# Kernel optimization log

Hardware: AMD Instinct MI355X
Metric: run time of the kernel (lower is better)

Reference implementation:

```python
import jax, jax.numpy as jnp
import numpy as np

EMBED = 256
B, S = 4, 4096

def _linear_params(key, d):
    k1, k2 = jax.random.split(key)
    lim = 1.0 / np.sqrt(d)
    W = jax.random.uniform(k1, (d, d), jnp.float32, -lim, lim)
    b = jax.random.uniform(k2, (d,), jnp.float32, -lim, lim)
    return W, b

def setup_inputs() -> dict:
    key = jax.random.key(0)
    ks = jax.random.split(key, 6)
    x = jax.random.normal(ks[0], (B, S, EMBED), jnp.float32)
    Wq, bq = _linear_params(ks[1], EMBED)
    Wk, bk = _linear_params(ks[2], EMBED)
    Wv, bv = _linear_params(ks[3], EMBED)
    Wl, bl = _linear_params(ks[4], EMBED)
    g1 = jnp.ones((EMBED,), jnp.float32); be1 = jnp.zeros((EMBED,), jnp.float32)
    g2 = jnp.ones((EMBED,), jnp.float32); be2 = jnp.zeros((EMBED,), jnp.float32)
    return {"x": x, "Wq": Wq, "bq": bq, "Wk": Wk, "bk": bk, "Wv": Wv, "bv": bv,
            "Wl": Wl, "bl": bl, "g1": g1, "be1": be1, "g2": g2, "be2": be2}

def _layernorm(x, g, b, eps=1e-5):
    mu = jnp.mean(x, axis=-1, keepdims=True)
    var = jnp.mean(jnp.square(x - mu), axis=-1, keepdims=True)
    return (x - mu) * jax.lax.rsqrt(var + eps) * g + b

def reference(x, Wq, bq, Wk, bk, Wv, bv, Wl, bl, g1, be1, g2, be2):
    d = x.shape[-1]
    q = jnp.einsum('bsd,ed->bse', x, Wq) + bq
    k = jnp.einsum('bsd,ed->bse', x, Wk) + bk
    v = jnp.einsum('bsd,ed->bse', x, Wv) + bv
    scores = jnp.einsum('bqd,bkd->bqk', q, k) / np.sqrt(d).astype(np.float32)
    attn = jax.nn.softmax(scores, axis=-1)
    out = jnp.einsum('bqk,bkd->bqd', attn, v)
    h = _layernorm(x + out, g1, be1)
    # NOTE: same linear applied twice (as in the original module)
    h = jnp.einsum('bsd,ed->bse', h, Wl) + bl
    h = jax.nn.relu(h)
    h = jnp.einsum('bsd,ed->bse', h, Wl) + bl
    return _layernorm(x + h, g2, be2)
```

## Files before the change

kernel.cpp:

```cpp
#include <hip/hip_runtime.h>

typedef unsigned short u16;
typedef float  f32x4 __attribute__((ext_vector_type(4)));
typedef short  s16x8 __attribute__((ext_vector_type(8)));
typedef unsigned short u16x4 __attribute__((ext_vector_type(4)));

__device__ __forceinline__ u16 f2b(float f) {
    unsigned b = __float_as_uint(f);
    return (u16)((b + 0x7FFFu + ((b >> 16) & 1u)) >> 16);
}
__device__ __forceinline__ float b2f(u16 u) { return __uint_as_float(((unsigned)u) << 16); }

__device__ __forceinline__ int perm64(int r) {
    return (r & 0x23) | (((r >> 2) & 3) << 3) | (((r >> 4) & 1) << 2);
}

__device__ __forceinline__ void gload16(const u16* g, u16* l) {
    __builtin_amdgcn_global_load_lds(
        (const __attribute__((address_space(1))) unsigned int*)g,
        (__attribute__((address_space(3))) unsigned int*)l,
        16, 0, 0);
}

__global__ __launch_bounds__(256) void cvt_f2b_k(const float* __restrict__ src, u16* __restrict__ dst, int n) {
    int i = (blockIdx.x * 256 + threadIdx.x) * 4;
    if (i < n) {
        f32x4 v = *(const f32x4*)(src + i);
        u16x4 o;
        o[0] = f2b(v[0]); o[1] = f2b(v[1]); o[2] = f2b(v[2]); o[3] = f2b(v[3]);
        *(u16x4*)(dst + i) = o;
    }
}

template<int TRANS, int RELU>
__global__ __launch_bounds__(256) void gemm_k256(const u16* __restrict__ A, const u16* __restrict__ W,
                                                 const float* __restrict__ bias, u16* __restrict__ Cd,
                                                 float scale) {
    const int tid = threadIdx.x;
    const int wv = tid >> 6, lane = tid & 63, g = lane >> 4, lq = lane & 15;
    const int m0 = blockIdx.x * 64, n0 = blockIdx.y * 64;

    const u16* arow = A + (size_t)(m0 + wv * 16 + lq) * 256;
    f32x4 acc[4];
#pragma unroll
    for (int nf = 0; nf < 4; ++nf) { acc[nf][0] = 0.f; acc[nf][1] = 0.f; acc[nf][2] = 0.f; acc[nf][3] = 0.f; }

#pragma unroll
    for (int kk = 0; kk < 8; ++kk) {
        s16x8 a = *(const s16x8*)(arow + kk * 32 + g * 8);
#pragma unroll
        for (int nf = 0; nf < 4; ++nf) {
            s16x8 b = *(const s16x8*)(W + (size_t)(n0 + nf * 16 + lq) * 256 + kk * 32 + g * 8);
            acc[nf] = __builtin_amdgcn_mfma_f32_16x16x32_bf16(a, b, acc[nf], 0, 0, 0);
        }
    }

    __shared__ __align__(16) u16 c_lds[64 * 64];
#pragma unroll
    for (int nf = 0; nf < 4; ++nf) {
        float bb = bias[n0 + nf * 16 + lq];
#pragma unroll
        for (int j = 0; j < 4; ++j) {
            float v = acc[nf][j] + bb;
            if (RELU) v = fmaxf(v, 0.f);
            v *= scale;
            if (!TRANS) c_lds[(wv * 16 + (g << 2) + j) * 64 + nf * 16 + lq] = f2b(v);
            else        c_lds[(nf * 16 + lq) * 64 + wv * 16 + (g << 2) + j] = f2b(v);
        }
    }
    __syncthreads();
    if (!TRANS) {
#pragma unroll
        for (int r = 0; r < 2; ++r) {
            int o = (r * 256 + tid) * 8, row = o >> 6, col = o & 63;
            *(s16x8*)(Cd + (size_t)(m0 + row) * 256 + n0 + col) = *(const s16x8*)(c_lds + row * 64 + col);
        }
    } else {
        int bidx = m0 >> 12, s0 = m0 & 4095;
#pragma unroll
        for (int r = 0; r < 2; ++r) {
            int o = (r * 256 + tid) * 8, drow = o >> 6, col = o & 63;
            *(s16x8*)(Cd + (size_t)bidx * 256 * 4096 + (size_t)(n0 + drow) * 4096 + s0 + col) =
                *(const s16x8*)(c_lds + drow * 64 + col);
        }
    }
}

__global__ __launch_bounds__(256, 1) void flash2(const u16* __restrict__ Q, const u16* __restrict__ K,
                                                 const u16* __restrict__ VT, u16* __restrict__ Opart,
                                                 float* __restrict__ ml) {
    __shared__ __align__(16) u16 smem[65536];
    const int tid = threadIdx.x;
    const int wv = tid >> 6, lane = tid & 63, g = lane >> 4, lqi = lane & 15;
    const int bx = blockIdx.x, s = blockIdx.y;
    const int b = bx >> 5, q0 = (bx & 31) << 7;
    const int kvbase = s * 2048;

    const u16* kb_ = K + (size_t)b * 4096 * 256;
    const u16* vb_ = VT + (size_t)b * 256 * 4096;

    s16x8 qf[2][8];
#pragma unroll
    for (int qh = 0; qh < 2; ++qh) {
        const u16* qrow = Q + (size_t)(b * 4096 + q0 + wv * 32 + qh * 16 + lqi) * 256;
#pragma unroll
        for (int kk = 0; kk < 8; ++kk) qf[qh][kk] = *(const s16x8*)(qrow + kk * 32 + g * 8);
    }

    int koff[8], voff[8];
#pragma unroll
    for (int r = 0; r < 8; ++r) {
        int row = r * 8 + (tid >> 5), ch = tid & 31;
        koff[r] = perm64(row) * 256 + ((ch ^ (row & 7)) << 3);
        int vrow = r * 32 + (tid >> 3), vch = tid & 7;
        voff[r] = vrow * 4096 + ((vch ^ (vrow & 7)) << 3);
    }

    f32x4 acc[2][16];
#pragma unroll
    for (int qh = 0; qh < 2; ++qh)
#pragma unroll
        for (int nf = 0; nf < 16; ++nf) { acc[qh][nf][0]=0.f; acc[qh][nf][1]=0.f; acc[qh][nf][2]=0.f; acc[qh][nf][3]=0.f; }
    float mrun[2] = {-1e30f, -1e30f}, lrun[2] = {0.f, 0.f};

    auto STAGE = [&](int bufsel, int t) {
        const u16* kt = kb_ + (size_t)(kvbase + (t << 6)) * 256;
        const u16* vt = vb_ + (kvbase + (t << 6));
        u16* kl = smem + bufsel * 32768 + tid * 8;
        u16* vl = kl + 16384;
#pragma unroll
        for (int r = 0; r < 8; ++r) gload16(kt + koff[r], kl + r * 2048);
#pragma unroll
        for (int r = 0; r < 8; ++r) gload16(vt + voff[r], vl + r * 2048);
    };

    auto COMPUTE = [&](int bufsel) {
        const u16* kbuf = smem + bufsel * 32768;
        const u16* vbuf = kbuf + 16384;
        f32x4 st[2][4];
#pragma unroll
        for (int qh = 0; qh < 2; ++qh)
#pragma unroll
            for (int f = 0; f < 4; ++f) { st[qh][f][0]=0.f; st[qh][f][1]=0.f; st[qh][f][2]=0.f; st[qh][f][3]=0.f; }
#pragma unroll
        for (int kk = 0; kk < 8; ++kk) {
#pragma unroll
            for (int f = 0; f < 4; ++f) {
                int row = f * 16 + lqi;
                s16x8 a = *(const s16x8*)(kbuf + ((row << 5) + (((kk << 2) + g) ^ (row & 7))) * 8);
                st[0][f] = __builtin_amdgcn_mfma_f32_16x16x32_bf16(a, qf[0][kk], st[0][f], 0, 0, 0);
                st[1][f] = __builtin_amdgcn_mfma_f32_16x16x32_bf16(a, qf[1][kk], st[1][f], 0, 0, 0);
            }
        }
        s16x8 pa[2][2];
#pragma unroll
        for (int qh = 0; qh < 2; ++qh) {
            float rm = -1e30f;
#pragma unroll
            for (int f = 0; f < 4; ++f)
                rm = fmaxf(rm, fmaxf(fmaxf(st[qh][f][0], st[qh][f][1]), fmaxf(st[qh][f][2], st[qh][f][3])));
            rm = fmaxf(rm, __shfl_xor(rm, 16));
            rm = fmaxf(rm, __shfl_xor(rm, 32));
            if (!__all(rm - mrun[qh] <= 8.f)) {
                float mnew = fmaxf(mrun[qh], rm);
                float alpha = exp2f(mrun[qh] - mnew);
#pragma unroll
                for (int j = 0; j < 4; ++j) {
                    float a4 = __shfl(alpha, (g << 2) + j);
#pragma unroll
                    for (int nf = 0; nf < 16; ++nf) acc[qh][nf][j] *= a4;
                }
                mrun[qh] = mnew;
                lrun[qh] *= alpha;
            }
            float ps = 0.f;
#pragma unroll
            for (int f = 0; f < 4; ++f)
#pragma unroll
                for (int j = 0; j < 4; ++j) { float e = exp2f(st[qh][f][j] - mrun[qh]); st[qh][f][j] = e; ps += e; }
            ps += __shfl_xor(ps, 16);
            ps += __shfl_xor(ps, 32);
            lrun[qh] += ps;
#pragma unroll
            for (int kk2 = 0; kk2 < 2; ++kk2) {
                union { s16x8 v; u16 u[8]; } pu;
#pragma unroll
                for (int j2 = 0; j2 < 4; ++j2) { pu.u[j2] = f2b(st[qh][2*kk2][j2]); pu.u[4+j2] = f2b(st[qh][2*kk2+1][j2]); }
                pa[qh][kk2] = pu.v;
            }
        }
#pragma unroll
        for (int kk2 = 0; kk2 < 2; ++kk2) {
#pragma unroll
            for (int nf = 0; nf < 16; ++nf) {
                int row = (nf << 4) + lqi;
                s16x8 bv = *(const s16x8*)(vbuf + ((row << 3) + (((kk2 << 2) + g) ^ (row & 7))) * 8);
                acc[0][nf] = __builtin_amdgcn_mfma_f32_16x16x32_bf16(pa[0][kk2], bv, acc[0][nf], 0, 0, 0);
                acc[1][nf] = __builtin_amdgcn_mfma_f32_16x16x32_bf16(pa[1][kk2], bv, acc[1][nf], 0, 0, 0);
            }
        }
    };

    STAGE(0, 0);
    for (int t2 = 0; t2 < 32; t2 += 2) {
        __syncthreads();
        STAGE(1, t2 + 1);
        COMPUTE(0);
        __syncthreads();
        if (t2 + 2 < 32) STAGE(0, t2 + 2);
        COMPUTE(1);
    }

    __syncthreads();
    float linv[2][4];
#pragma unroll
    for (int qh = 0; qh < 2; ++qh)
#pragma unroll
        for (int j = 0; j < 4; ++j) linv[qh][j] = 1.0f / __shfl(lrun[qh], (g << 2) + j);
    u16* o_lds = smem;
#pragma unroll
    for (int qh = 0; qh < 2; ++qh)
#pragma unroll
        for (int nf = 0; nf < 16; ++nf)
#pragma unroll
            for (int j = 0; j < 4; ++j)
                o_lds[(wv * 32 + qh * 16 + (g << 2) + j) * 256 + (nf << 4) + lqi] = f2b(acc[qh][nf][j] * linv[qh][j]);
    __syncthreads();
    u16* orow = Opart + (size_t)s * 4194304 + (size_t)(b * 4096 + q0) * 256;
#pragma unroll
    for (int r = 0; r < 16; ++r) {
        int o = (r * 256 + tid) * 8, row = o >> 8, col = o & 255;
        *(s16x8*)(orow + (size_t)row * 256 + col) = *(const s16x8*)(o_lds + row * 256 + col);
    }
    if (lane < 16) {
#pragma unroll
        for (int qh = 0; qh < 2; ++qh) {
            int grow = b * 4096 + q0 + wv * 32 + qh * 16 + lqi;
            ml[s * 32768 + grow]         = mrun[qh];
            ml[s * 32768 + 16384 + grow] = lrun[qh];
        }
    }
}

__global__ __launch_bounds__(256) void recomb_k(const u16* __restrict__ Opart, const float* __restrict__ ml,
                                                u16* __restrict__ out) {
    const int row = blockIdx.x * 4 + (threadIdx.x >> 6);
    const int lane = threadIdx.x & 63;
    float m0 = ml[row],          l0 = ml[16384 + row];
    float m1 = ml[32768 + row],  l1 = ml[49152 + row];
    float mm = fmaxf(m0, m1);
    float a0 = l0 * exp2f(m0 - mm), a1 = l1 * exp2f(m1 - mm);
    float rs = 1.0f / (a0 + a1);
    a0 *= rs; a1 *= rs;
    u16x4 v0 = *(const u16x4*)(Opart + (size_t)row * 256 + lane * 4);
    u16x4 v1 = *(const u16x4*)(Opart + 4194304 + (size_t)row * 256 + lane * 4);
    u16x4 o;
#pragma unroll
    for (int i = 0; i < 4; ++i) o[i] = f2b(a0 * b2f(v0[i]) + a1 * b2f(v1[i]));
    *(u16x4*)(out + (size_t)row * 256 + lane * 4) = o;
}

template<int OUTF32>
__global__ __launch_bounds__(256) void ln_k(const float* __restrict__ x, const u16* __restrict__ add,
                                            const float* __restrict__ gam, const float* __restrict__ bet,
                                            float* __restrict__ outf, u16* __restrict__ outb) {
    const int row = blockIdx.x * 4 + (threadIdx.x >> 6);
    const int lane = threadIdx.x & 63;
    f32x4 xv = *(const f32x4*)(x + (size_t)row * 256 + lane * 4);
    u16x4 av = *(const u16x4*)(add + (size_t)row * 256 + lane * 4);
    float s[4];
#pragma unroll
    for (int i = 0; i < 4; ++i) s[i] = xv[i] + b2f(av[i]);
    float sum = s[0] + s[1] + s[2] + s[3];
    float sq = s[0] * s[0] + s[1] * s[1] + s[2] * s[2] + s[3] * s[3];
#pragma unroll
    for (int d = 1; d < 64; d <<= 1) { sum += __shfl_xor(sum, d); sq += __shfl_xor(sq, d); }
    float mean = sum * (1.f / 256.f);
    float var = sq * (1.f / 256.f) - mean * mean;
    float rstd = rsqrtf(var + 1e-5f);
    f32x4 gv = *(const f32x4*)(gam + lane * 4);
    f32x4 bv = *(const f32x4*)(bet + lane * 4);
    if (OUTF32) {
        f32x4 y;
#pragma unroll
        for (int i = 0; i < 4; ++i) y[i] = (s[i] - mean) * rstd * gv[i] + bv[i];
        *(f32x4*)(outf + (size_t)row * 256 + lane * 4) = y;
    } else {
        u16x4 y;
#pragma unroll
        for (int i = 0; i < 4; ++i) y[i] = f2b((s[i] - mean) * rstd * gv[i] + bv[i]);
        *(u16x4*)(outb + (size_t)row * 256 + lane * 4) = y;
    }
}

extern "C" void kernel_launch(void* const* d_in, const int* in_sizes, int n_in,
                              void* d_out, int out_size, void* d_ws, size_t ws_size,
                              hipStream_t stream) {
    const float* x   = (const float*)d_in[0];
    const float* Wq  = (const float*)d_in[1];
    const float* bq  = (const float*)d_in[2];
    const float* Wk  = (const float*)d_in[3];
    const float* bk  = (const float*)d_in[4];
    const float* Wv  = (const float*)d_in[5];
    const float* bv  = (const float*)d_in[6];
    const float* Wl  = (const float*)d_in[7];
    const float* bl  = (const float*)d_in[8];
    const float* g1  = (const float*)d_in[9];
    const float* be1 = (const float*)d_in[10];
    const float* g2  = (const float*)d_in[11];
    const float* be2 = (const float*)d_in[12];
    float* out = (float*)d_out;

    const size_t NT = 16384 * 256;
    u16* xb  = (u16*)d_ws;
    u16* qb  = xb  + NT;
    u16* kb  = qb  + NT;
    u16* vtb = kb  + NT;
    u16* o01 = vtb + NT;
    u16* wqb = o01 + 2 * NT;
    u16* wkb = wqb + 65536;
    u16* wvb = wkb + 65536;
    u16* wlb = wvb + 65536;
    float* ml = (float*)(wlb + 65536);

    cvt_f2b_k<<<4096, 256, 0, stream>>>(x, xb, 4194304);
    cvt_f2b_k<<<64, 256, 0, stream>>>(Wq, wqb, 65536);
    cvt_f2b_k<<<64, 256, 0, stream>>>(Wk, wkb, 65536);
    cvt_f2b_k<<<64, 256, 0, stream>>>(Wv, wvb, 65536);
    cvt_f2b_k<<<64, 256, 0, stream>>>(Wl, wlb, 65536);

    dim3 ggrid(256, 4);
    gemm_k256<0, 0><<<ggrid, 256, 0, stream>>>(xb, wqb, bq, qb, 0.0625f * 1.44269504f);
    gemm_k256<0, 0><<<ggrid, 256, 0, stream>>>(xb, wkb, bk, kb, 1.0f);
    gemm_k256<1, 0><<<ggrid, 256, 0, stream>>>(xb, wvb, bv, vtb, 1.0f);

    flash2<<<dim3(128, 2), 256, 0, stream>>>(qb, kb, vtb, o01, ml);
    recomb_k<<<4096, 256, 0, stream>>>(o01, ml, xb );

    ln_k<0><<<4096, 256, 0, stream>>>(x, xb, g1, be1, nullptr, qb );

    gemm_k256<0, 1><<<ggrid, 256, 0, stream>>>(qb, wlb, bl, kb , 1.0f);
    gemm_k256<0, 0><<<ggrid, 256, 0, stream>>>(kb, wlb, bl, vtb , 1.0f);

    ln_k<1><<<4096, 256, 0, stream>>>(x, vtb, g2, be2, out, nullptr);
}
```

Measured before the change: 371.1 us.

## Fuse QKV projection with x conversion, widen flash blocks, add split-K variants

```diff
diff --git a/kernel.cpp b/kernel.cpp
--- a/kernel.cpp
+++ b/kernel.cpp
@@ -4,6 +4,8 @@
 typedef float  f32x4 __attribute__((ext_vector_type(4)));
 typedef short  s16x8 __attribute__((ext_vector_type(8)));
 typedef unsigned short u16x4 __attribute__((ext_vector_type(4)));
+
+#define NT 4194304
 
 __device__ __forceinline__ u16 f2b(float f) {
     unsigned b = __float_as_uint(f);
@@ -22,29 +24,95 @@
         16, 0, 0);
 }
 
-__global__ __launch_bounds__(256) void cvt_f2b_k(const float* __restrict__ src, u16* __restrict__ dst, int n) {
+__global__ __launch_bounds__(256) void cvt_w4(const float* __restrict__ w0, const float* __restrict__ w1,
+                                              const float* __restrict__ w2, const float* __restrict__ w3,
+                                              u16* __restrict__ dst) {
+    const int z = blockIdx.y;
+    const float* src = z == 0 ? w0 : z == 1 ? w1 : z == 2 ? w2 : w3;
     int i = (blockIdx.x * 256 + threadIdx.x) * 4;
-    if (i < n) {
-        f32x4 v = *(const f32x4*)(src + i);
-        u16x4 o;
-        o[0] = f2b(v[0]); o[1] = f2b(v[1]); o[2] = f2b(v[2]); o[3] = f2b(v[3]);
-        *(u16x4*)(dst + i) = o;
-    }
-}
-
-template<int TRANS, int RELU>
+    f32x4 v = *(const f32x4*)(src + i);
+    u16x4 o;
+    o[0] = f2b(v[0]); o[1] = f2b(v[1]); o[2] = f2b(v[2]); o[3] = f2b(v[3]);
+    *(u16x4*)(dst + (size_t)z * 65536 + i) = o;
+}
+
+__global__ __launch_bounds__(256) void gemm_qkv(const float* __restrict__ x, const u16* __restrict__ wqkv,
+                                                const float* __restrict__ bq, const float* __restrict__ bk,
+                                                const float* __restrict__ bv,
+                                                u16* __restrict__ q, u16* __restrict__ k, u16* __restrict__ vt,
+                                                float qscale) {
+    const int tid = threadIdx.x;
+    const int wid = tid >> 6, lane = tid & 63, g = lane >> 4, lq = lane & 15;
+    const int m0 = blockIdx.x * 64, n0 = blockIdx.y * 64, z = blockIdx.z;
+    const u16* W = wqkv + (size_t)z * 65536;
+    const float* bias = z == 0 ? bq : z == 1 ? bk : bv;
+    const float scale = z == 0 ? qscale : 1.0f;
+
+    const float* arow = x + (size_t)(m0 + wid * 16 + lq) * 256;
+    s16x8 af[8];
+#pragma unroll
+    for (int kk = 0; kk < 8; ++kk) {
+        f32x4 lo = *(const f32x4*)(arow + kk * 32 + g * 8);
+        f32x4 hi = *(const f32x4*)(arow + kk * 32 + g * 8 + 4);
+        union { s16x8 v; u16 u[8]; } pu;
+#pragma unroll
+        for (int e = 0; e < 4; ++e) { pu.u[e] = f2b(lo[e]); pu.u[4 + e] = f2b(hi[e]); }
+        af[kk] = pu.v;
+    }
+
+    f32x4 acc[4];
+#pragma unroll
+    for (int nf = 0; nf < 4; ++nf) { acc[nf][0]=0.f; acc[nf][1]=0.f; acc[nf][2]=0.f; acc[nf][3]=0.f; }
+#pragma unroll
+    for (int kk = 0; kk < 8; ++kk) {
+#pragma unroll
+        for (int nf = 0; nf < 4; ++nf) {
+            s16x8 b = *(const s16x8*)(W + (size_t)(n0 + nf * 16 + lq) * 256 + kk * 32 + g * 8);
+            acc[nf] = __builtin_amdgcn_mfma_f32_16x16x32_bf16(af[kk], b, acc[nf], 0, 0, 0);
+        }
+    }
+
+    __shared__ __align__(16) u16 c_lds[64 * 64];
+#pragma unroll
+    for (int nf = 0; nf < 4; ++nf) {
+        float bb = bias[n0 + nf * 16 + lq];
+#pragma unroll
+        for (int j = 0; j < 4; ++j) {
+            float v = (acc[nf][j] + bb) * scale;
+            if (z != 2) c_lds[(wid * 16 + (g << 2) + j) * 64 + nf * 16 + lq] = f2b(v);
+            else        c_lds[(nf * 16 + lq) * 64 + wid * 16 + (g << 2) + j] = f2b(v);
+        }
+    }
+    __syncthreads();
+    if (z != 2) {
+        u16* Cd = z == 0 ? q : k;
+#pragma unroll
+        for (int r = 0; r < 2; ++r) {
+            int o = (r * 256 + tid) * 8, row = o >> 6, col = o & 63;
+            *(s16x8*)(Cd + (size_t)(m0 + row) * 256 + n0 + col) = *(const s16x8*)(c_lds + row * 64 + col);
+        }
+    } else {
+        int bidx = m0 >> 12, s0 = m0 & 4095;
+#pragma unroll
+        for (int r = 0; r < 2; ++r) {
+            int o = (r * 256 + tid) * 8, drow = o >> 6, col = o & 63;
+            *(s16x8*)(vt + (size_t)bidx * 1048576 + (size_t)(n0 + drow) * 4096 + s0 + col) =
+                *(const s16x8*)(c_lds + drow * 64 + col);
+        }
+    }
+}
+
+template<int RELU>
 __global__ __launch_bounds__(256) void gemm_k256(const u16* __restrict__ A, const u16* __restrict__ W,
-                                                 const float* __restrict__ bias, u16* __restrict__ Cd,
-                                                 float scale) {
+                                                 const float* __restrict__ bias, u16* __restrict__ Cd) {
     const int tid = threadIdx.x;
-    const int wv = tid >> 6, lane = tid & 63, g = lane >> 4, lq = lane & 15;
+    const int wid = tid >> 6, lane = tid & 63, g = lane >> 4, lq = lane & 15;
     const int m0 = blockIdx.x * 64, n0 = blockIdx.y * 64;
 
-    const u16* arow = A + (size_t)(m0 + wv * 16 + lq) * 256;
+    const u16* arow = A + (size_t)(m0 + wid * 16 + lq) * 256;
     f32x4 acc[4];
 #pragma unroll
-    for (int nf = 0; nf < 4; ++nf) { acc[nf][0] = 0.f; acc[nf][1] = 0.f; acc[nf][2] = 0.f; acc[nf][3] = 0.f; }
-
+    for (int nf = 0; nf < 4; ++nf) { acc[nf][0]=0.f; acc[nf][1]=0.f; acc[nf][2]=0.f; acc[nf][3]=0.f; }
 #pragma unroll
     for (int kk = 0; kk < 8; ++kk) {
         s16x8 a = *(const s16x8*)(arow + kk * 32 + g * 8);
@@ -54,7 +122,6 @@
             acc[nf] = __builtin_amdgcn_mfma_f32_16x16x32_bf16(a, b, acc[nf], 0, 0, 0);
         }
     }
-
     __shared__ __align__(16) u16 c_lds[64 * 64];
 #pragma unroll
     for (int nf = 0; nf < 4; ++nf) {
@@ -63,38 +130,25 @@
         for (int j = 0; j < 4; ++j) {
             float v = acc[nf][j] + bb;
             if (RELU) v = fmaxf(v, 0.f);
-            v *= scale;
-            if (!TRANS) c_lds[(wv * 16 + (g << 2) + j) * 64 + nf * 16 + lq] = f2b(v);
-            else        c_lds[(nf * 16 + lq) * 64 + wv * 16 + (g << 2) + j] = f2b(v);
+            c_lds[(wid * 16 + (g << 2) + j) * 64 + nf * 16 + lq] = f2b(v);
         }
     }
     __syncthreads();
-    if (!TRANS) {
-#pragma unroll
-        for (int r = 0; r < 2; ++r) {
-            int o = (r * 256 + tid) * 8, row = o >> 6, col = o & 63;
-            *(s16x8*)(Cd + (size_t)(m0 + row) * 256 + n0 + col) = *(const s16x8*)(c_lds + row * 64 + col);
-        }
-    } else {
-        int bidx = m0 >> 12, s0 = m0 & 4095;
-#pragma unroll
-        for (int r = 0; r < 2; ++r) {
-            int o = (r * 256 + tid) * 8, drow = o >> 6, col = o & 63;
-            *(s16x8*)(Cd + (size_t)bidx * 256 * 4096 + (size_t)(n0 + drow) * 4096 + s0 + col) =
-                *(const s16x8*)(c_lds + drow * 64 + col);
-        }
-    }
-}
-
-__global__ __launch_bounds__(256, 1) void flash2(const u16* __restrict__ Q, const u16* __restrict__ K,
+#pragma unroll
+    for (int r = 0; r < 2; ++r) {
+        int o = (r * 256 + tid) * 8, row = o >> 6, col = o & 63;
+        *(s16x8*)(Cd + (size_t)(m0 + row) * 256 + n0 + col) = *(const s16x8*)(c_lds + row * 64 + col);
+    }
+}
+
+__global__ __launch_bounds__(512, 2) void flash3(const u16* __restrict__ Q, const u16* __restrict__ K,
                                                  const u16* __restrict__ VT, u16* __restrict__ Opart,
-                                                 float* __restrict__ ml) {
+                                                 float* __restrict__ ml, int ntiles) {
     __shared__ __align__(16) u16 smem[65536];
     const int tid = threadIdx.x;
-    const int wv = tid >> 6, lane = tid & 63, g = lane >> 4, lqi = lane & 15;
-    const int bx = blockIdx.x, s = blockIdx.y;
-    const int b = bx >> 5, q0 = (bx & 31) << 7;
-    const int kvbase = s * 2048;
+    const int wid = tid >> 6, lane = tid & 63, g = lane >> 4, lqi = lane & 15;
+    const int b = blockIdx.x >> 4, q0 = (blockIdx.x & 15) << 8;
+    const int s = blockIdx.y, kvbase = s * (ntiles << 6);
 
     const u16* kb_ = K + (size_t)b * 4096 * 256;
     const u16* vb_ = VT + (size_t)b * 256 * 4096;
@@ -102,17 +156,18 @@
     s16x8 qf[2][8];
 #pragma unroll
     for (int qh = 0; qh < 2; ++qh) {
-        const u16* qrow = Q + (size_t)(b * 4096 + q0 + wv * 32 + qh * 16 + lqi) * 256;
+        const u16* qrow = Q + (size_t)(b * 4096 + q0 + wid * 32 + qh * 16 + lqi) * 256;
 #pragma unroll
         for (int kk = 0; kk < 8; ++kk) qf[qh][kk] = *(const s16x8*)(qrow + kk * 32 + g * 8);
     }
 
-    int koff[8], voff[8];
-#pragma unroll
-    for (int r = 0; r < 8; ++r) {
-        int row = r * 8 + (tid >> 5), ch = tid & 31;
+    int koff[4], voff[4];
+#pragma unroll
+    for (int r = 0; r < 4; ++r) {
+        int c = r * 512 + tid;
+        int row = c >> 5, ch = c & 31;
         koff[r] = perm64(row) * 256 + ((ch ^ (row & 7)) << 3);
-        int vrow = r * 32 + (tid >> 3), vch = tid & 7;
+        int vrow = c >> 3, vch = c & 7;
         voff[r] = vrow * 4096 + ((vch ^ (vrow & 7)) << 3);
     }
 
@@ -126,12 +181,12 @@
     auto STAGE = [&](int bufsel, int t) {
         const u16* kt = kb_ + (size_t)(kvbase + (t << 6)) * 256;
         const u16* vt = vb_ + (kvbase + (t << 6));
-        u16* kl = smem + bufsel * 32768 + tid * 8;
+        u16* kl = smem + bufsel * 32768;
         u16* vl = kl + 16384;
 #pragma unroll
-        for (int r = 0; r < 8; ++r) gload16(kt + koff[r], kl + r * 2048);
-#pragma unroll
-        for (int r = 0; r < 8; ++r) gload16(vt + voff[r], vl + r * 2048);
+        for (int r = 0; r < 4; ++r) gload16(kt + koff[r], kl + (r * 512 + tid) * 8);
+#pragma unroll
+        for (int r = 0; r < 4; ++r) gload16(vt + voff[r], vl + (r * 512 + tid) * 8);
     };
 
     auto COMPUTE = [&](int bufsel) {
@@ -142,6 +197,7 @@
         for (int qh = 0; qh < 2; ++qh)
 #pragma unroll
             for (int f = 0; f < 4; ++f) { st[qh][f][0]=0.f; st[qh][f][1]=0.f; st[qh][f][2]=0.f; st[qh][f][3]=0.f; }
+        __builtin_amdgcn_s_setprio(1);
 #pragma unroll
         for (int kk = 0; kk < 8; ++kk) {
 #pragma unroll
@@ -152,6 +208,7 @@
                 st[1][f] = __builtin_amdgcn_mfma_f32_16x16x32_bf16(a, qf[1][kk], st[1][f], 0, 0, 0);
             }
         }
+        __builtin_amdgcn_s_setprio(0);
         s16x8 pa[2][2];
 #pragma unroll
         for (int qh = 0; qh < 2; ++qh) {
@@ -189,6 +246,7 @@
                 pa[qh][kk2] = pu.v;
             }
         }
+        __builtin_amdgcn_s_setprio(1);
 #pragma unroll
         for (int kk2 = 0; kk2 < 2; ++kk2) {
 #pragma unroll
@@ -199,15 +257,16 @@
                 acc[1][nf] = __builtin_amdgcn_mfma_f32_16x16x32_bf16(pa[1][kk2], bv, acc[1][nf], 0, 0, 0);
             }
         }
+        __builtin_amdgcn_s_setprio(0);
     };
 
     STAGE(0, 0);
-    for (int t2 = 0; t2 < 32; t2 += 2) {
+    for (int t2 = 0; t2 < ntiles; t2 += 2) {
         __syncthreads();
         STAGE(1, t2 + 1);
         COMPUTE(0);
         __syncthreads();
-        if (t2 + 2 < 32) STAGE(0, t2 + 2);
+        if (t2 + 2 < ntiles) STAGE(0, t2 + 2);
         COMPUTE(1);
     }
 
@@ -224,39 +283,47 @@
         for (int nf = 0; nf < 16; ++nf)
 #pragma unroll
             for (int j = 0; j < 4; ++j)
-                o_lds[(wv * 32 + qh * 16 + (g << 2) + j) * 256 + (nf << 4) + lqi] = f2b(acc[qh][nf][j] * linv[qh][j]);
+                o_lds[(wid * 32 + qh * 16 + (g << 2) + j) * 256 + (nf << 4) + lqi] = f2b(acc[qh][nf][j] * linv[qh][j]);
     __syncthreads();
-    u16* orow = Opart + (size_t)s * 4194304 + (size_t)(b * 4096 + q0) * 256;
+    u16* orow = Opart + (size_t)s * NT + (size_t)(b * 4096 + q0) * 256;
 #pragma unroll
     for (int r = 0; r < 16; ++r) {
-        int o = (r * 256 + tid) * 8, row = o >> 8, col = o & 255;
+        int o = (r * 512 + tid) * 8, row = o >> 8, col = o & 255;
         *(s16x8*)(orow + (size_t)row * 256 + col) = *(const s16x8*)(o_lds + row * 256 + col);
     }
     if (lane < 16) {
 #pragma unroll
         for (int qh = 0; qh < 2; ++qh) {
-            int grow = b * 4096 + q0 + wv * 32 + qh * 16 + lqi;
+            int grow = b * 4096 + q0 + wid * 32 + qh * 16 + lqi;
             ml[s * 32768 + grow]         = mrun[qh];
             ml[s * 32768 + 16384 + grow] = lrun[qh];
         }
     }
 }
 
+template<int S>
 __global__ __launch_bounds__(256) void recomb_k(const u16* __restrict__ Opart, const float* __restrict__ ml,
                                                 u16* __restrict__ out) {
     const int row = blockIdx.x * 4 + (threadIdx.x >> 6);
     const int lane = threadIdx.x & 63;
-    float m0 = ml[row],          l0 = ml[16384 + row];
-    float m1 = ml[32768 + row],  l1 = ml[49152 + row];
-    float mm = fmaxf(m0, m1);
-    float a0 = l0 * exp2f(m0 - mm), a1 = l1 * exp2f(m1 - mm);
-    float rs = 1.0f / (a0 + a1);
-    a0 *= rs; a1 *= rs;
-    u16x4 v0 = *(const u16x4*)(Opart + (size_t)row * 256 + lane * 4);
-    u16x4 v1 = *(const u16x4*)(Opart + 4194304 + (size_t)row * 256 + lane * 4);
-    u16x4 o;
-#pragma unroll
-    for (int i = 0; i < 4; ++i) o[i] = f2b(a0 * b2f(v0[i]) + a1 * b2f(v1[i]));
+    float m[S], l[S];
+#pragma unroll
+    for (int s = 0; s < S; ++s) { m[s] = ml[s * 32768 + row]; l[s] = ml[s * 32768 + 16384 + row]; }
+    float mm = m[0];
+#pragma unroll
+    for (int s = 1; s < S; ++s) mm = fmaxf(mm, m[s]);
+    float a[S], tot = 0.f;
+#pragma unroll
+    for (int s = 0; s < S; ++s) { a[s] = l[s] * exp2f(m[s] - mm); tot += a[s]; }
+    float rs = 1.0f / tot;
+    float r0 = 0.f, r1 = 0.f, r2 = 0.f, r3 = 0.f;
+#pragma unroll
+    for (int s = 0; s < S; ++s) {
+        float w = a[s] * rs;
+        u16x4 v = *(const u16x4*)(Opart + (size_t)s * NT + (size_t)row * 256 + lane * 4);
+        r0 += w * b2f(v[0]); r1 += w * b2f(v[1]); r2 += w * b2f(v[2]); r3 += w * b2f(v[3]);
+    }
+    u16x4 o; o[0] = f2b(r0); o[1] = f2b(r1); o[2] = f2b(r2); o[3] = f2b(r3);
     *(u16x4*)(out + (size_t)row * 256 + lane * 4) = o;
 }
 
@@ -272,7 +339,7 @@
 #pragma unroll
     for (int i = 0; i < 4; ++i) s[i] = xv[i] + b2f(av[i]);
     float sum = s[0] + s[1] + s[2] + s[3];
-    float sq = s[0] * s[0] + s[1] * s[1] + s[2] * s[2] + s[3] * s[3];
+    float sq = s[0]*s[0] + s[1]*s[1] + s[2]*s[2] + s[3]*s[3];
 #pragma unroll
     for (int d = 1; d < 64; d <<= 1) { sum += __shfl_xor(sum, d); sq += __shfl_xor(sq, d); }
     float mean = sum * (1.f / 256.f);
@@ -311,36 +378,34 @@
     const float* be2 = (const float*)d_in[12];
     float* out = (float*)d_out;
 
-    const size_t NT = 16384 * 256;
-    u16* xb  = (u16*)d_ws;
-    u16* qb  = xb  + NT;
-    u16* kb  = qb  + NT;
-    u16* vtb = kb  + NT;
-    u16* o01 = vtb + NT;
-    u16* wqb = o01 + 2 * NT;
-    u16* wkb = wqb + 65536;
-    u16* wvb = wkb + 65536;
-    u16* wlb = wvb + 65536;
+    u16* qb   = (u16*)d_ws;
+    u16* kb   = qb + NT;
+    u16* vtb  = kb + NT;
+    u16* op   = vtb + NT;
+
+    const size_t need4 = ((size_t)7 * NT + 4 * 65536) * 2 + 4 * 32768 * 4;
+    const int SPLITS = (ws_size >= need4) ? 4 : 2;
+
+    u16* wqkv = op + (size_t)SPLITS * NT;
+    u16* wlb  = wqkv + 3 * 65536;
     float* ml = (float*)(wlb + 65536);
 
-    cvt_f2b_k<<<4096, 256, 0, stream>>>(x, xb, 4194304);
-    cvt_f2b_k<<<64, 256, 0, stream>>>(Wq, wqb, 65536);
-    cvt_f2b_k<<<64, 256, 0, stream>>>(Wk, wkb, 65536);
-    cvt_f2b_k<<<64, 256, 0, stream>>>(Wv, wvb, 65536);
-    cvt_f2b_k<<<64, 256, 0, stream>>>(Wl, wlb, 65536);
+    cvt_w4<<<dim3(64, 4), 256, 0, stream>>>(Wq, Wk, Wv, Wl, wqkv);
+
+    gemm_qkv<<<dim3(256, 4, 3), 256, 0, stream>>>(x, wqkv, bq, bk, bv, qb, kb, vtb,
+                                                  0.0625f * 1.44269504f);
+
+    const int ntiles = 4096 / (64 * SPLITS);
+    flash3<<<dim3(64, SPLITS), 512, 0, stream>>>(qb, kb, vtb, op, ml, ntiles);
+
+    if (SPLITS == 4) recomb_k<4><<<4096, 256, 0, stream>>>(op, ml, qb);
+    else             recomb_k<2><<<4096, 256, 0, stream>>>(op, ml, qb);
+
+    ln_k<0><<<4096, 256, 0, stream>>>(x, qb, g1, be1, nullptr, kb );
 
     dim3 ggrid(256, 4);
-    gemm_k256<0, 0><<<ggrid, 256, 0, stream>>>(xb, wqb, bq, qb, 0.0625f * 1.44269504f);
-    gemm_k256<0, 0><<<ggrid, 256, 0, stream>>>(xb, wkb, bk, kb, 1.0f);
-    gemm_k256<1, 0><<<ggrid, 256, 0, stream>>>(xb, wvb, bv, vtb, 1.0f);
-
-    flash2<<<dim3(128, 2), 256, 0, stream>>>(qb, kb, vtb, o01, ml);
-    recomb_k<<<4096, 256, 0, stream>>>(o01, ml, xb );
-
-    ln_k<0><<<4096, 256, 0, stream>>>(x, xb, g1, be1, nullptr, qb );
-
-    gemm_k256<0, 1><<<ggrid, 256, 0, stream>>>(qb, wlb, bl, kb , 1.0f);
-    gemm_k256<0, 0><<<ggrid, 256, 0, stream>>>(kb, wlb, bl, vtb , 1.0f);
-
-    ln_k<1><<<4096, 256, 0, stream>>>(x, vtb, g2, be2, out, nullptr);
-}
+    gemm_k256<1><<<ggrid, 256, 0, stream>>>(kb, wlb, bl, vtb );
+    gemm_k256<0><<<ggrid, 256, 0, stream>>>(vtb, wlb, bl, op );
+
+    ln_k<1><<<4096, 256, 0, stream>>>(x, op, g2, be2, out, nullptr);
+}
```

Result: slower. 514.7 us (+38.7%).
